# Performance work log

Hardware: AMD Instinct MI355X
Metric: run time of the kernel (lower is better)

Reference implementation:

```python
import jax, jax.numpy as jnp
import numpy as np

EPS = 1e-12

def _ff_degree(x, w_in, scale, bias, w_out):
    # x: [b, n, d, m]; w_in: [d, h]; scale/bias: [1, 1, h]; w_out: [h, d]
    h = jnp.einsum('bndm,dh->bnhm', x, w_in)
    norm = jnp.clip(jnp.linalg.norm(h, axis=-1, keepdims=True), EPS, None)  # [b,n,h,1]
    phase = h / norm
    gated = jax.nn.gelu(norm[..., 0] * scale + bias, approximate=False)[..., None]
    h = gated * phase
    return jnp.einsum('bnhm,hd->bndm', h, w_out)


def setup_inputs() -> dict:
    key = jax.random.key(0)
    ks = jax.random.split(key, 16)
    b, n, dim, mult = 4, 4096, 256, 4
    hid = dim * mult
    degrees = [0, 1, 2]
    inp = {}
    for i, deg in enumerate(degrees):
        m = 2 * deg + 1
        inp[f'x{deg}'] = jax.random.normal(ks[i], (b, n, dim, m), dtype=jnp.float32)
        inp[f'w_in{deg}'] = jax.random.normal(ks[3 + i], (dim, hid), dtype=jnp.float32) / np.sqrt(dim)
        inp[f'scale{deg}'] = jnp.ones((1, 1, hid), dtype=jnp.float32)
        inp[f'bias{deg}'] = jax.random.uniform(ks[6 + i], (1, 1, hid), dtype=jnp.float32, minval=-0.001, maxval=0.001)
        inp[f'w_out{deg}'] = jax.random.normal(ks[9 + i], (hid, dim), dtype=jnp.float32) / np.sqrt(hid)
    return inp


def reference(x0, x1, x2,
              w_in0, scale0, bias0, w_out0,
              w_in1, scale1, bias1, w_out1,
              w_in2, scale2, bias2, w_out2):
    y0 = _ff_degree(x0, w_in0, scale0, bias0, w_out0)
    y1 = _ff_degree(x1, w_in1, scale1, bias1, w_out1)
    y2 = _ff_degree(x2, w_in2, scale2, bias2, w_out2)
    return (y0, y1, y2)
```

## Files before the change

### kernel.cpp

```cpp
#include <hip/hip_runtime.h>
#include <hip/hip_bf16.h>


typedef __attribute__((ext_vector_type(8))) short short8;
typedef __attribute__((ext_vector_type(4))) float f32x4;

static __device__ __forceinline__ short f2bf(float f) {
  __hip_bfloat16 h = __float2bfloat16(f);
  return *reinterpret_cast<short*>(&h);
}

__global__ void pack_all_k(const float* __restrict__ w0i, const float* __restrict__ w0o,
                           const float* __restrict__ w1i, const float* __restrict__ w1o,
                           const float* __restrict__ w2i, const float* __restrict__ w2o,
                           short* __restrict__ p) {
  const int region = blockIdx.x >> 7;
  const int gid = (blockIdx.x & 127) * 256 + threadIdx.x;
  const int lane = gid & 63;
  const int tile = gid >> 6;
  const int gg = lane >> 4, cc = lane & 15;
  const float* w = (region == 0) ? w0i : (region == 1) ? w0o :
                   (region == 2) ? w1i : (region == 3) ? w1o :
                   (region == 4) ? w2i : w2o;
  short8 v;
  if (region & 1) {
    const int nt2 = tile & 15, kt2 = tile >> 4;
#pragma unroll
    for (int j = 0; j < 8; ++j)
      v[j] = f2bf(w[(kt2 * 32 + gg * 8 + j) * 256 + nt2 * 16 + cc]);
  } else {
    const int kt = tile & 7, nt = tile >> 3;
#pragma unroll
    for (int j = 0; j < 8; ++j)
      v[j] = f2bf(w[(kt * 32 + gg * 8 + j) * 1024 + nt * 16 + cc]);
  }
  *reinterpret_cast<short8*>(p + ((size_t)region * 262144) + gid * 8) = v;
}

template<int NT, int GRP, int OUT_M>
__global__ __launch_bounds__(256, 2)
void ff_se3_kernel(const float* __restrict__ x,
                   const short* __restrict__ wpin,
                   const short* __restrict__ wpout,
                   const float* __restrict__ scale,
                   const float* __restrict__ bias,
                   float* __restrict__ out)
{
  constexpr int T = 16 * NT;
  constexpr int R = (OUT_M == 1) ? T : 16;
  extern __shared__ short lds[];
  short* lA  = lds;
  short* lH0 = lds + T * 256;
  short* lH1 = lH0 + T * 128;

  const int tid  = threadIdx.x;
  const int lane = tid & 63;
  const int wave = tid >> 6;
  const int g    = lane >> 4;
  const int lc   = lane & 15;
  const long row0 = (long)blockIdx.x * R;

  for (int e4 = tid; e4 < R * 64 * OUT_M; e4 += 256) {
    const int r  = e4 / (64 * OUT_M);
    const int o4 = e4 - r * (64 * OUT_M);
    const f32x4 v = __builtin_nontemporal_load(
        reinterpret_cast<const f32x4*>(x + (row0 + r) * (256 * OUT_M) + o4 * 4));
#pragma unroll
    for (int i = 0; i < 4; ++i) {
      const int flat = o4 * 4 + i;
      const int d  = flat / OUT_M;
      const int mm = flat - d * OUT_M;
      const int t  = mm * 16 + r;
      const int byte = t * 512 + ((d * 2) ^ ((t & 7) << 4));
      lA[byte >> 1] = f2bf(v[i]);
    }
  }

  f32x4 acc_out[NT][4];
#pragma unroll
  for (int a = 0; a < NT; ++a)
#pragma unroll
    for (int b = 0; b < 4; ++b) acc_out[a][b] = (f32x4)(0.f);

  __syncthreads();

  for (int c = 0; c < 8; ++c) {
    short* lH = (c & 1) ? lH1 : lH0;

    float sc2[2], bi2[2];
#pragma unroll
    for (int nn = 0; nn < 2; ++nn) {
      const int hgl = c * 128 + wave * 32 + nn * 16 + lc;
      sc2[nn] = scale[hgl];
      bi2[nn] = bias[hgl];
    }

    f32x4 acc1[NT][2];
#pragma unroll
    for (int a = 0; a < NT; ++a) { acc1[a][0] = (f32x4)(0.f); acc1[a][1] = (f32x4)(0.f); }
#pragma unroll
    for (int kt = 0; kt < 8; ++kt) {
      short8 af[NT];
#pragma unroll
      for (int a = 0; a < NT; ++a) {
        const int t = a * 16 + lc;
        const int byte = t * 512 + (((kt * 32 + g * 8) * 2) ^ ((t & 7) << 4));
        af[a] = *reinterpret_cast<const short8*>(&lA[byte >> 1]);
      }
      short8 bfr[2];
#pragma unroll
      for (int nn = 0; nn < 2; ++nn) {
        const int ntg = c * 8 + wave * 2 + nn;
        bfr[nn] = *reinterpret_cast<const short8*>(wpin + ((ntg * 8 + kt) * 64 + lane) * 8);
      }
#pragma unroll
      for (int a = 0; a < NT; ++a)
#pragma unroll
        for (int nn = 0; nn < 2; ++nn)
          acc1[a][nn] = __builtin_amdgcn_mfma_f32_16x16x32_bf16(af[a], bfr[nn], acc1[a][nn], 0, 0, 0);
    }

    short8 b2p[4][4];
#pragma unroll
    for (int kk = 0; kk < 4; ++kk)
#pragma unroll
      for (int nn = 0; nn < 4; ++nn) {
        const int tile = (c * 4 + kk) * 16 + wave * 4 + nn;
        b2p[kk][nn] = *reinterpret_cast<const short8*>(wpout + (tile * 64 + lane) * 8);
      }

#pragma unroll
    for (int nn = 0; nn < 2; ++nn) {
      const float sc = sc2[nn];
      const float bi = bi2[nn];
#pragma unroll
      for (int reg = 0; reg < 4; ++reg) {
#pragma unroll
        for (int gi = 0; gi < NT / GRP; ++gi) {
          float ns = 0.f;
#pragma unroll
          for (int k = 0; k < GRP; ++k) {
            const float h = acc1[gi * GRP + k][nn][reg];
            ns += h * h;
          }
          ns = fmaxf(ns, 1e-24f);
          const float rn  = __builtin_amdgcn_rsqf(ns);
          const float nrm = ns * rn;
          const float z   = fmaf(nrm, sc, bi);
          float u2 = 2.f * z * fmaf(0.0356774081f * z, z, 0.7978845608f);
          u2 = fminf(u2, 30.f);
          const float e  = __expf(u2);
          const float th = (e - 1.f) * __builtin_amdgcn_rcpf(e + 1.f);
          const float fac = 0.5f * (1.f + th) * z * rn;
          const int tl  = g * 4 + reg;
          const int col = wave * 32 + nn * 16 + lc;
#pragma unroll
          for (int k = 0; k < GRP; ++k) {
            const int a = gi * GRP + k;
            const int t = a * 16 + tl;
            const int byte = t * 256 + ((col * 2) ^ ((t & 7) << 4));
            lH[byte >> 1] = f2bf(acc1[a][nn][reg] * fac);
          }
        }
      }
    }

    __syncthreads();

#pragma unroll
    for (int kk = 0; kk < 4; ++kk) {
      short8 a2[NT];
#pragma unroll
      for (int a = 0; a < NT; ++a) {
        const int t = a * 16 + lc;
        const int byte = t * 256 + (((kk * 32 + g * 8) * 2) ^ ((t & 7) << 4));
        a2[a] = *reinterpret_cast<const short8*>(&lH[byte >> 1]);
      }
#pragma unroll
      for (int a = 0; a < NT; ++a)
#pragma unroll
        for (int nn = 0; nn < 4; ++nn)
          acc_out[a][nn] = __builtin_amdgcn_mfma_f32_16x16x32_bf16(a2[a], b2p[kk][nn], acc_out[a][nn], 0, 0, 0);
    }
  }

  __syncthreads();
  float* ldsF = reinterpret_cast<float*>(lds);
  constexpr int RW = 256 * OUT_M;
  if constexpr (OUT_M == 1) {
#pragma unroll
    for (int a = 0; a < NT; ++a)
#pragma unroll
      for (int nn = 0; nn < 4; ++nn) {
        const int d = wave * 64 + nn * 16 + lc;
#pragma unroll
        for (int reg = 0; reg < 4; ++reg) {
          const int t = a * 16 + g * 4 + reg;
          ldsF[t * RW + d] = acc_out[a][nn][reg];
        }
      }
  } else {
#pragma unroll
    for (int mm = 0; mm < NT; ++mm)
#pragma unroll
      for (int nn = 0; nn < 4; ++nn) {
        const int d = wave * 64 + nn * 16 + lc;
#pragma unroll
        for (int reg = 0; reg < 4; ++reg) {
          const int r = g * 4 + reg;
          ldsF[r * RW + d * OUT_M + mm] = acc_out[mm][nn][reg];
        }
      }
  }
  __syncthreads();
  float* obase = out + row0 * RW;
  constexpr int NF4 = (R * RW) / 4;
  for (int i = tid; i < NF4; i += 256) {
    const f32x4 v = *reinterpret_cast<const f32x4*>(&ldsF[i * 4]);
    __builtin_nontemporal_store(v, reinterpret_cast<f32x4*>(obase) + i);
  }
}

extern "C" void kernel_launch(void* const* d_in, const int* in_sizes, int n_in,
                              void* d_out, int out_size, void* d_ws, size_t ws_size,
                              hipStream_t stream)
{
  short* ws = (short*)d_ws;
  const size_t WSZ = 262144;
  float* outf = (float*)d_out;
  const size_t out_off[3] = {0, 4194304, 16777216};

  pack_all_k<<<768, 256, 0, stream>>>(
      (const float*)d_in[1],  (const float*)d_in[4],
      (const float*)d_in[6],  (const float*)d_in[9],
      (const float*)d_in[11], (const float*)d_in[14], ws);

  for (int dg = 0; dg < 3; ++dg) {
    const float* x  = (const float*)d_in[5 * dg + 0];
    const float* sc = (const float*)d_in[5 * dg + 2];
    const float* bi = (const float*)d_in[5 * dg + 3];
    const short* pin  = ws + (2 * dg) * WSZ;
    const short* pout = ws + (2 * dg + 1) * WSZ;
    float* o = outf + out_off[dg];
    switch (dg) {
      case 0:
        ff_se3_kernel<2, 1, 1><<<512, 256, 32768, stream>>>(x, pin, pout, sc, bi, o);
        break;
      case 1:
        ff_se3_kernel<3, 3, 3><<<1024, 256, 49152, stream>>>(x, pin, pout, sc, bi, o);
        break;
      case 2:
        ff_se3_kernel<5, 5, 5><<<1024, 256, 81920, stream>>>(x, pin, pout, sc, bi, o);
        break;
    }
  }
}
```

Measured before the change: 266.8 us.

## Split per-block work across eight waves instead of four

Doubles the block size to 512 threads and gives each wave half the hidden columns in the first GEMM and half the output columns in the second GEMM. This halves the per-wave accumulator and B-fragment register footprint so more waves can hide latency. The cost is that each wave re-reads the same A fragments from LDS, roughly doubling LDS read traffic, and barriers now cover more waves. The launch bound asks for four blocks per CU, but LDS size (up to 80 KB per block) will likely cap occupancy below that.

```diff
diff --git a/kernel.cpp b/kernel.cpp
--- a/kernel.cpp
+++ b/kernel.cpp
@@ -38,7 +38,7 @@
 }
 
 template<int NT, int GRP, int OUT_M>
-__global__ __launch_bounds__(256, 2)
+__global__ __launch_bounds__(512, 4)
 void ff_se3_kernel(const float* __restrict__ x,
                    const short* __restrict__ wpin,
                    const short* __restrict__ wpout,
@@ -60,7 +60,7 @@
   const int lc   = lane & 15;
   const long row0 = (long)blockIdx.x * R;
 
-  for (int e4 = tid; e4 < R * 64 * OUT_M; e4 += 256) {
+  for (int e4 = tid; e4 < R * 64 * OUT_M; e4 += 512) {
     const int r  = e4 / (64 * OUT_M);
     const int o4 = e4 - r * (64 * OUT_M);
     const f32x4 v = __builtin_nontemporal_load(
@@ -76,28 +76,22 @@
     }
   }
 
-  f32x4 acc_out[NT][4];
-#pragma unroll
-  for (int a = 0; a < NT; ++a)
-#pragma unroll
-    for (int b = 0; b < 4; ++b) acc_out[a][b] = (f32x4)(0.f);
+  f32x4 acc_out[NT][2];
+#pragma unroll
+  for (int a = 0; a < NT; ++a) { acc_out[a][0] = (f32x4)(0.f); acc_out[a][1] = (f32x4)(0.f); }
 
   __syncthreads();
 
   for (int c = 0; c < 8; ++c) {
     short* lH = (c & 1) ? lH1 : lH0;
 
-    float sc2[2], bi2[2];
-#pragma unroll
-    for (int nn = 0; nn < 2; ++nn) {
-      const int hgl = c * 128 + wave * 32 + nn * 16 + lc;
-      sc2[nn] = scale[hgl];
-      bi2[nn] = bias[hgl];
-    }
-
-    f32x4 acc1[NT][2];
-#pragma unroll
-    for (int a = 0; a < NT; ++a) { acc1[a][0] = (f32x4)(0.f); acc1[a][1] = (f32x4)(0.f); }
+    const int hgl = c * 128 + wave * 16 + lc;
+    const float sc = scale[hgl];
+    const float bi = bias[hgl];
+
+    f32x4 acc1[NT];
+#pragma unroll
+    for (int a = 0; a < NT; ++a) acc1[a] = (f32x4)(0.f);
 #pragma unroll
     for (int kt = 0; kt < 8; ++kt) {
       short8 af[NT];
@@ -107,60 +101,49 @@
         const int byte = t * 512 + (((kt * 32 + g * 8) * 2) ^ ((t & 7) << 4));
         af[a] = *reinterpret_cast<const short8*>(&lA[byte >> 1]);
       }
-      short8 bfr[2];
+      const int ntg = c * 8 + wave;
+      const short8 bfr = *reinterpret_cast<const short8*>(wpin + ((ntg * 8 + kt) * 64 + lane) * 8);
+#pragma unroll
+      for (int a = 0; a < NT; ++a)
+        acc1[a] = __builtin_amdgcn_mfma_f32_16x16x32_bf16(af[a], bfr, acc1[a], 0, 0, 0);
+    }
+
+    short8 b2p[4][2];
+#pragma unroll
+    for (int kk = 0; kk < 4; ++kk)
 #pragma unroll
       for (int nn = 0; nn < 2; ++nn) {
-        const int ntg = c * 8 + wave * 2 + nn;
-        bfr[nn] = *reinterpret_cast<const short8*>(wpin + ((ntg * 8 + kt) * 64 + lane) * 8);
-      }
-#pragma unroll
-      for (int a = 0; a < NT; ++a)
-#pragma unroll
-        for (int nn = 0; nn < 2; ++nn)
-          acc1[a][nn] = __builtin_amdgcn_mfma_f32_16x16x32_bf16(af[a], bfr[nn], acc1[a][nn], 0, 0, 0);
-    }
-
-    short8 b2p[4][4];
-#pragma unroll
-    for (int kk = 0; kk < 4; ++kk)
-#pragma unroll
-      for (int nn = 0; nn < 4; ++nn) {
-        const int tile = (c * 4 + kk) * 16 + wave * 4 + nn;
+        const int tile = (c * 4 + kk) * 16 + wave * 2 + nn;
         b2p[kk][nn] = *reinterpret_cast<const short8*>(wpout + (tile * 64 + lane) * 8);
       }
 
 #pragma unroll
-    for (int nn = 0; nn < 2; ++nn) {
-      const float sc = sc2[nn];
-      const float bi = bi2[nn];
-#pragma unroll
-      for (int reg = 0; reg < 4; ++reg) {
-#pragma unroll
-        for (int gi = 0; gi < NT / GRP; ++gi) {
-          float ns = 0.f;
-#pragma unroll
-          for (int k = 0; k < GRP; ++k) {
-            const float h = acc1[gi * GRP + k][nn][reg];
-            ns += h * h;
-          }
-          ns = fmaxf(ns, 1e-24f);
-          const float rn  = __builtin_amdgcn_rsqf(ns);
-          const float nrm = ns * rn;
-          const float z   = fmaf(nrm, sc, bi);
-          float u2 = 2.f * z * fmaf(0.0356774081f * z, z, 0.7978845608f);
-          u2 = fminf(u2, 30.f);
-          const float e  = __expf(u2);
-          const float th = (e - 1.f) * __builtin_amdgcn_rcpf(e + 1.f);
-          const float fac = 0.5f * (1.f + th) * z * rn;
-          const int tl  = g * 4 + reg;
-          const int col = wave * 32 + nn * 16 + lc;
-#pragma unroll
-          for (int k = 0; k < GRP; ++k) {
-            const int a = gi * GRP + k;
-            const int t = a * 16 + tl;
-            const int byte = t * 256 + ((col * 2) ^ ((t & 7) << 4));
-            lH[byte >> 1] = f2bf(acc1[a][nn][reg] * fac);
-          }
+    for (int reg = 0; reg < 4; ++reg) {
+#pragma unroll
+      for (int gi = 0; gi < NT / GRP; ++gi) {
+        float ns = 0.f;
+#pragma unroll
+        for (int k = 0; k < GRP; ++k) {
+          const float h = acc1[gi * GRP + k][reg];
+          ns += h * h;
+        }
+        ns = fmaxf(ns, 1e-24f);
+        const float rn  = __builtin_amdgcn_rsqf(ns);
+        const float nrm = ns * rn;
+        const float z   = fmaf(nrm, sc, bi);
+        float u2 = 2.f * z * fmaf(0.0356774081f * z, z, 0.7978845608f);
+        u2 = fminf(u2, 30.f);
+        const float e  = __expf(u2);
+        const float th = (e - 1.f) * __builtin_amdgcn_rcpf(e + 1.f);
+        const float fac = 0.5f * (1.f + th) * z * rn;
+        const int tl  = g * 4 + reg;
+        const int col = wave * 16 + lc;
+#pragma unroll
+        for (int k = 0; k < GRP; ++k) {
+          const int a = gi * GRP + k;
+          const int t = a * 16 + tl;
+          const int byte = t * 256 + ((col * 2) ^ ((t & 7) << 4));
+          lH[byte >> 1] = f2bf(acc1[a][reg] * fac);
         }
       }
     }
@@ -179,7 +162,7 @@
 #pragma unroll
       for (int a = 0; a < NT; ++a)
 #pragma unroll
-        for (int nn = 0; nn < 4; ++nn)
+        for (int nn = 0; nn < 2; ++nn)
           acc_out[a][nn] = __builtin_amdgcn_mfma_f32_16x16x32_bf16(a2[a], b2p[kk][nn], acc_out[a][nn], 0, 0, 0);
     }
   }
@@ -191,8 +174,8 @@
 #pragma unroll
     for (int a = 0; a < NT; ++a)
 #pragma unroll
-      for (int nn = 0; nn < 4; ++nn) {
-        const int d = wave * 64 + nn * 16 + lc;
+      for (int nn = 0; nn < 2; ++nn) {
+        const int d = wave * 32 + nn * 16 + lc;
 #pragma unroll
         for (int reg = 0; reg < 4; ++reg) {
           const int t = a * 16 + g * 4 + reg;
@@ -203,8 +186,8 @@
 #pragma unroll
     for (int mm = 0; mm < NT; ++mm)
 #pragma unroll
-      for (int nn = 0; nn < 4; ++nn) {
-        const int d = wave * 64 + nn * 16 + lc;
+      for (int nn = 0; nn < 2; ++nn) {
+        const int d = wave * 32 + nn * 16 + lc;
 #pragma unroll
         for (int reg = 0; reg < 4; ++reg) {
           const int r = g * 4 + reg;
@@ -215,7 +198,7 @@
   __syncthreads();
   float* obase = out + row0 * RW;
   constexpr int NF4 = (R * RW) / 4;
-  for (int i = tid; i < NF4; i += 256) {
+  for (int i = tid; i < NF4; i += 512) {
     const f32x4 v = *reinterpret_cast<const f32x4*>(&ldsF[i * 4]);
     __builtin_nontemporal_store(v, reinterpret_cast<f32x4*>(obase) + i);
   }
@@ -244,13 +227,13 @@
     float* o = outf + out_off[dg];
     switch (dg) {
       case 0:
-        ff_se3_kernel<2, 1, 1><<<512, 256, 32768, stream>>>(x, pin, pout, sc, bi, o);
+        ff_se3_kernel<2, 1, 1><<<512, 512, 32768, stream>>>(x, pin, pout, sc, bi, o);
         break;
       case 1:
-        ff_se3_kernel<3, 3, 3><<<1024, 256, 49152, stream>>>(x, pin, pout, sc, bi, o);
+        ff_se3_kernel<3, 3, 3><<<1024, 512, 49152, stream>>>(x, pin, pout, sc, bi, o);
         break;
       case 2:
-        ff_se3_kernel<5, 5, 5><<<1024, 256, 81920, stream>>>(x, pin, pout, sc, bi, o);
+        ff_se3_kernel<5, 5, 5><<<1024, 512, 81920, stream>>>(x, pin, pout, sc, bi, o);
         break;
     }
   }
```

Measured after the change: 231.6 us. 1.15x faster.

## Use 512-thread blocks with wider hidden chunks and direct global loads for degree 0

Applied to the files above, without the earlier changes.

Blocks grow to 8 waves, each owning a narrower output-column slice. The hidden dimension is processed in 4 chunks of 256 instead of 8 chunks of 128, with a single LDS hidden buffer and an extra barrier in place of double buffering. The degree-0 kernel skips LDS staging of x and converts fp32 rows from global memory straight into MFMA fragments, while w_out fragments are now loaded per k-step instead of prefetched up front. The aim is fewer chunk iterations and barriers per row tile and more waves to hide latency. In exchange, __launch_bounds__(512,4) tightens the register budget and may cause spills, the larger LDS footprint limits occupancy for higher degrees, and the extra barrier adds synchronisation.

```diff
diff --git a/kernel.cpp b/kernel.cpp
--- a/kernel.cpp
+++ b/kernel.cpp
@@ -37,8 +37,8 @@
   *reinterpret_cast<short8*>(p + ((size_t)region * 262144) + gid * 8) = v;
 }
 
-template<int NT, int GRP, int OUT_M>
-__global__ __launch_bounds__(256, 2)
+template<int NT, int GRP, int OUT_M, int MODE>
+__global__ __launch_bounds__(512, 4)
 void ff_se3_kernel(const float* __restrict__ x,
                    const short* __restrict__ wpin,
                    const short* __restrict__ wpout,
@@ -49,9 +49,8 @@
   constexpr int T = 16 * NT;
   constexpr int R = (OUT_M == 1) ? T : 16;
   extern __shared__ short lds[];
-  short* lA  = lds;
-  short* lH0 = lds + T * 256;
-  short* lH1 = lH0 + T * 128;
+  short* lA = lds;
+  short* lH = (MODE == 0) ? (lds + T * 256) : lds;
 
   const int tid  = threadIdx.x;
   const int lane = tid & 63;
@@ -60,37 +59,35 @@
   const int lc   = lane & 15;
   const long row0 = (long)blockIdx.x * R;
 
-  for (int e4 = tid; e4 < R * 64 * OUT_M; e4 += 256) {
-    const int r  = e4 / (64 * OUT_M);
-    const int o4 = e4 - r * (64 * OUT_M);
-    const f32x4 v = __builtin_nontemporal_load(
-        reinterpret_cast<const f32x4*>(x + (row0 + r) * (256 * OUT_M) + o4 * 4));
-#pragma unroll
-    for (int i = 0; i < 4; ++i) {
-      const int flat = o4 * 4 + i;
-      const int d  = flat / OUT_M;
-      const int mm = flat - d * OUT_M;
-      const int t  = mm * 16 + r;
-      const int byte = t * 512 + ((d * 2) ^ ((t & 7) << 4));
-      lA[byte >> 1] = f2bf(v[i]);
-    }
-  }
-
-  f32x4 acc_out[NT][4];
-#pragma unroll
-  for (int a = 0; a < NT; ++a)
-#pragma unroll
-    for (int b = 0; b < 4; ++b) acc_out[a][b] = (f32x4)(0.f);
-
-  __syncthreads();
-
-  for (int c = 0; c < 8; ++c) {
-    short* lH = (c & 1) ? lH1 : lH0;
-
+  if constexpr (MODE == 0) {
+    for (int e4 = tid; e4 < R * 64 * OUT_M; e4 += 512) {
+      const int r  = e4 / (64 * OUT_M);
+      const int o4 = e4 - r * (64 * OUT_M);
+      const f32x4 v = __builtin_nontemporal_load(
+          reinterpret_cast<const f32x4*>(x + (row0 + r) * (256 * OUT_M) + o4 * 4));
+#pragma unroll
+      for (int i = 0; i < 4; ++i) {
+        const int flat = o4 * 4 + i;
+        const int d  = flat / OUT_M;
+        const int mm = flat - d * OUT_M;
+        const int t  = mm * 16 + r;
+        const int byte = t * 512 + ((d * 2) ^ ((t & 7) << 4));
+        lA[byte >> 1] = f2bf(v[i]);
+      }
+    }
+  }
+
+  f32x4 acc_out[NT][2];
+#pragma unroll
+  for (int a = 0; a < NT; ++a) { acc_out[a][0] = (f32x4)(0.f); acc_out[a][1] = (f32x4)(0.f); }
+
+  if constexpr (MODE == 0) __syncthreads();
+
+  for (int c = 0; c < 4; ++c) {
     float sc2[2], bi2[2];
 #pragma unroll
     for (int nn = 0; nn < 2; ++nn) {
-      const int hgl = c * 128 + wave * 32 + nn * 16 + lc;
+      const int hgl = c * 256 + wave * 32 + nn * 16 + lc;
       sc2[nn] = scale[hgl];
       bi2[nn] = bias[hgl];
     }
@@ -103,14 +100,24 @@
       short8 af[NT];
 #pragma unroll
       for (int a = 0; a < NT; ++a) {
-        const int t = a * 16 + lc;
-        const int byte = t * 512 + (((kt * 32 + g * 8) * 2) ^ ((t & 7) << 4));
-        af[a] = *reinterpret_cast<const short8*>(&lA[byte >> 1]);
+        if constexpr (MODE == 0) {
+          const int t = a * 16 + lc;
+          const int byte = t * 512 + (((kt * 32 + g * 8) * 2) ^ ((t & 7) << 4));
+          af[a] = *reinterpret_cast<const short8*>(&lA[byte >> 1]);
+        } else {
+          const float* xp = x + (((size_t)blockIdx.x * 32 + a * 16 + lc) * 256 + kt * 32 + g * 8);
+          const f32x4 p0 = *reinterpret_cast<const f32x4*>(xp);
+          const f32x4 p1 = *reinterpret_cast<const f32x4*>(xp + 4);
+          short8 t8;
+#pragma unroll
+          for (int j = 0; j < 4; ++j) { t8[j] = f2bf(p0[j]); t8[4 + j] = f2bf(p1[j]); }
+          af[a] = t8;
+        }
       }
       short8 bfr[2];
 #pragma unroll
       for (int nn = 0; nn < 2; ++nn) {
-        const int ntg = c * 8 + wave * 2 + nn;
+        const int ntg = c * 16 + wave * 2 + nn;
         bfr[nn] = *reinterpret_cast<const short8*>(wpin + ((ntg * 8 + kt) * 64 + lane) * 8);
       }
 #pragma unroll
@@ -120,14 +127,7 @@
           acc1[a][nn] = __builtin_amdgcn_mfma_f32_16x16x32_bf16(af[a], bfr[nn], acc1[a][nn], 0, 0, 0);
     }
 
-    short8 b2p[4][4];
-#pragma unroll
-    for (int kk = 0; kk < 4; ++kk)
-#pragma unroll
-      for (int nn = 0; nn < 4; ++nn) {
-        const int tile = (c * 4 + kk) * 16 + wave * 4 + nn;
-        b2p[kk][nn] = *reinterpret_cast<const short8*>(wpout + (tile * 64 + lane) * 8);
-      }
+    __syncthreads();
 
 #pragma unroll
     for (int nn = 0; nn < 2; ++nn) {
@@ -158,7 +158,7 @@
           for (int k = 0; k < GRP; ++k) {
             const int a = gi * GRP + k;
             const int t = a * 16 + tl;
-            const int byte = t * 256 + ((col * 2) ^ ((t & 7) << 4));
+            const int byte = t * 512 + ((col * 2) ^ ((t & 7) << 4));
             lH[byte >> 1] = f2bf(acc1[a][nn][reg] * fac);
           }
         }
@@ -168,19 +168,25 @@
     __syncthreads();
 
 #pragma unroll
-    for (int kk = 0; kk < 4; ++kk) {
+    for (int kk = 0; kk < 8; ++kk) {
       short8 a2[NT];
 #pragma unroll
       for (int a = 0; a < NT; ++a) {
         const int t = a * 16 + lc;
-        const int byte = t * 256 + (((kk * 32 + g * 8) * 2) ^ ((t & 7) << 4));
+        const int byte = t * 512 + (((kk * 32 + g * 8) * 2) ^ ((t & 7) << 4));
         a2[a] = *reinterpret_cast<const short8*>(&lH[byte >> 1]);
       }
+      short8 b2[2];
+#pragma unroll
+      for (int nn = 0; nn < 2; ++nn) {
+        const int tile = (c * 8 + kk) * 16 + wave * 2 + nn;
+        b2[nn] = *reinterpret_cast<const short8*>(wpout + (tile * 64 + lane) * 8);
+      }
 #pragma unroll
       for (int a = 0; a < NT; ++a)
 #pragma unroll
-        for (int nn = 0; nn < 4; ++nn)
-          acc_out[a][nn] = __builtin_amdgcn_mfma_f32_16x16x32_bf16(a2[a], b2p[kk][nn], acc_out[a][nn], 0, 0, 0);
+        for (int nn = 0; nn < 2; ++nn)
+          acc_out[a][nn] = __builtin_amdgcn_mfma_f32_16x16x32_bf16(a2[a], b2[nn], acc_out[a][nn], 0, 0, 0);
     }
   }
 
@@ -191,8 +197,8 @@
 #pragma unroll
     for (int a = 0; a < NT; ++a)
 #pragma unroll
-      for (int nn = 0; nn < 4; ++nn) {
-        const int d = wave * 64 + nn * 16 + lc;
+      for (int nn = 0; nn < 2; ++nn) {
+        const int d = wave * 32 + nn * 16 + lc;
 #pragma unroll
         for (int reg = 0; reg < 4; ++reg) {
           const int t = a * 16 + g * 4 + reg;
@@ -203,8 +209,8 @@
 #pragma unroll
     for (int mm = 0; mm < NT; ++mm)
 #pragma unroll
-      for (int nn = 0; nn < 4; ++nn) {
-        const int d = wave * 64 + nn * 16 + lc;
+      for (int nn = 0; nn < 2; ++nn) {
+        const int d = wave * 32 + nn * 16 + lc;
 #pragma unroll
         for (int reg = 0; reg < 4; ++reg) {
           const int r = g * 4 + reg;
@@ -215,7 +221,7 @@
   __syncthreads();
   float* obase = out + row0 * RW;
   constexpr int NF4 = (R * RW) / 4;
-  for (int i = tid; i < NF4; i += 256) {
+  for (int i = tid; i < NF4; i += 512) {
     const f32x4 v = *reinterpret_cast<const f32x4*>(&ldsF[i * 4]);
     __builtin_nontemporal_store(v, reinterpret_cast<f32x4*>(obase) + i);
   }
@@ -235,23 +241,15 @@
       (const float*)d_in[6],  (const float*)d_in[9],
       (const float*)d_in[11], (const float*)d_in[14], ws);
 
-  for (int dg = 0; dg < 3; ++dg) {
-    const float* x  = (const float*)d_in[5 * dg + 0];
-    const float* sc = (const float*)d_in[5 * dg + 2];
-    const float* bi = (const float*)d_in[5 * dg + 3];
-    const short* pin  = ws + (2 * dg) * WSZ;
-    const short* pout = ws + (2 * dg + 1) * WSZ;
-    float* o = outf + out_off[dg];
-    switch (dg) {
-      case 0:
-        ff_se3_kernel<2, 1, 1><<<512, 256, 32768, stream>>>(x, pin, pout, sc, bi, o);
-        break;
-      case 1:
-        ff_se3_kernel<3, 3, 3><<<1024, 256, 49152, stream>>>(x, pin, pout, sc, bi, o);
-        break;
-      case 2:
-        ff_se3_kernel<5, 5, 5><<<1024, 256, 81920, stream>>>(x, pin, pout, sc, bi, o);
-        break;
-    }
-  }
-}
+  ff_se3_kernel<2, 1, 1, 2><<<512, 512, 32768, stream>>>(
+      (const float*)d_in[0], ws + 0 * WSZ, ws + 1 * WSZ,
+      (const float*)d_in[2], (const float*)d_in[3], outf + out_off[0]);
+
+  ff_se3_kernel<3, 3, 3, 0><<<1024, 512, 49152, stream>>>(
+      (const float*)d_in[5], ws + 2 * WSZ, ws + 3 * WSZ,
+      (const float*)d_in[7], (const float*)d_in[8], outf + out_off[1]);
+
+  ff_se3_kernel<5, 5, 5, 0><<<1024, 512, 81920, stream>>>(
+      (const float*)d_in[10], ws + 4 * WSZ, ws + 5 * WSZ,
+      (const float*)d_in[12], (const float*)d_in[13], outf + out_off[2]);
+}
```

New measurement: 426.0 us. 1.6x slower.
